# Kernel tuning notes

Hardware: AMD Instinct MI355X
Metric: run time of the kernel (lower is better)

Reference implementation:

```python
import jax, jax.numpy as jnp
import numpy as np

RADIUS = 0.1
DILATION = 0.05
KERNEL_SIZE = 3  # per dim, ndim=3 -> ncells=27
NDIM = 3


def _cell_offsets():
    # Kernel cell center offsets relative to the query location.
    idx = jnp.stack(jnp.meshgrid(*([jnp.arange(KERNEL_SIZE)] * NDIM), indexing='ij'), axis=-1)
    idx = idx.reshape(-1, NDIM).astype(jnp.float32)  # [ncells, D]
    return (idx - (KERNEL_SIZE - 1) / 2.0) * DILATION


def setup_inputs() -> dict:
    key = jax.random.key(0)
    k1, k2, k3, k4, k5, k6 = jax.random.split(key, 6)
    B, N, M, K, C, O = 2, 8192, 8192, 32, 16, 16
    ncells = KERNEL_SIZE ** NDIM
    qlocs = jax.random.uniform(k1, (B, M, NDIM), dtype=jnp.float32)
    locs = jax.random.uniform(k2, (B, N, NDIM), dtype=jnp.float32)
    data = jax.random.normal(k3, (B, N, C), dtype=jnp.float32)
    neighbors = jax.random.randint(k4, (B, M, K), 0, N, dtype=jnp.int32)
    weight = jax.random.normal(k5, (O, C, ncells), dtype=jnp.float32) * 0.1
    bias = jax.random.normal(k6, (O,), dtype=jnp.float32) * 0.1
    return {"qlocs": qlocs, "locs": locs, "data": data,
            "neighbors": neighbors, "weight": weight, "bias": bias}


def reference(qlocs, locs, data, neighbors, weight, bias):
    # qlocs: [B,M,D], locs: [B,N,D], data: [B,N,C]
    # neighbors: [B,M,K] (-1 padded), weight: [O,C,ncells], bias: [O]
    valid = neighbors >= 0                      # [B,M,K]
    nid = jnp.where(valid, neighbors, 0)
    # Gather neighbor locations/features per batch.
    nlocs = jax.vmap(lambda l, n: l[n])(locs, nid)   # [B,M,K,D]
    ndata = jax.vmap(lambda d, n: d[n])(data, nid)   # [B,M,K,C]

    off = _cell_offsets()                            # [ncells, D]
    # Cell centers around each query point: [B,M,ncells,D]
    centers = qlocs[:, :, None, :] + off[None, None, :, :]
    # Distance from each cell center to each neighbor: [B,M,ncells,K]
    diff = centers[:, :, :, None, :] - nlocs[:, :, None, :, :]
    d = jnp.sqrt(jnp.sum(diff * diff, axis=-1) + 1e-12)
    q = d / RADIUS
    # 'default' SPH smoothing kernel: compact support, (1 - d/H)^3 inside radius.
    kv = jnp.where((q < 1.0) & valid[:, :, None, :], (1.0 - q) ** 3, 0.0)  # [B,M,ncells,K]

    # Per-cell SPH-weighted feature accumulation: [B,M,C,ncells]
    acc = jnp.einsum('bmek,bmkc->bmce', kv, ndata)
    # Contract with conv weights: [B,M,O]
    out = jnp.einsum('bmce,oce->bmo', acc, weight) + bias[None, None, :]
    return out
```

## Files before the change

kernel.cpp:

```cpp
#include <hip/hip_runtime.h>
#include <math.h>

#define NP 8192
#define KN 32
#define CH 16
#define OCH 16
#define NCELL 27
#define EPAD 36

#define THR2 0.0349f

__global__ __launch_bounds__(1024, 8) void convsp_kernel(
    const float* __restrict__ qlocs,
    const float* __restrict__ locs,
    const float* __restrict__ data,
    const int*   __restrict__ neighbors,
    const float* __restrict__ weight,
    const float* __restrict__ bias,
    float* __restrict__ out)
{
    __shared__ float  wlds[OCH * CH * EPAD];
    __shared__ float4 offs4[32];

    const int tid  = threadIdx.x;
    const int lane = tid & 63;
    const int c    = lane & 15;
    const int h    = lane >> 4;
    const int pt   = blockIdx.x * 16 + (tid >> 6);
    const int b    = pt >> 13;

    int   nid = neighbors[pt * KN + (lane & 31)];
    float qx = qlocs[pt * 3 + 0];
    float qy = qlocs[pt * 3 + 1];
    float qz = qlocs[pt * 3 + 2];

    for (int idx = tid; idx < OCH * CH * NCELL; idx += 1024) {
        int row = idx / NCELL;
        int e   = idx - row * NCELL;
        wlds[row * EPAD + e] = weight[idx];
    }
    for (int idx = tid; idx < OCH * CH * 9; idx += 1024) {
        int row = idx / 9;
        int e   = 27 + (idx - row * 9);
        wlds[row * EPAD + e] = 0.0f;
    }
    if (tid < 32) {
        int e = tid;
        float ox = (e < NCELL) ? (float)(e / 9 - 1) * 0.05f : 0.0f;
        float oy = (e < NCELL) ? (float)((e / 3) % 3 - 1) * 0.05f : 0.0f;
        float oz = (e < NCELL) ? (float)(e % 3 - 1) * 0.05f : 0.0f;
        offs4[tid] = make_float4(ox, oy, oz, 0.0f);
    }

    int gaddr = (b * NP + max(nid, 0)) * 3;
    float lx = locs[gaddr], ly = locs[gaddr + 1], lz = locs[gaddr + 2];

    __syncthreads();

    float dx = qx - lx, dy = qy - ly, dz = qz - lz;
    bool hit = (nid >= 0) && (dx * dx + dy * dy + dz * dz < THR2);
    unsigned int mask = (unsigned int)__ballot(hit);

    float acc[8];
    #pragma unroll
    for (int i = 0; i < 8; ++i) acc[i] = 0.0f;

    const float4* otab = &offs4[h * 8];

    unsigned int mrem = mask;
    while (mrem) {
        int k = __builtin_ctz(mrem);
        mrem &= mrem - 1;

        int   nk = __shfl(nid, k, 64);
        float nx = __shfl(lx,  k, 64);
        float ny = __shfl(ly,  k, 64);
        float nz = __shfl(lz,  k, 64);

        float ndc = data[(b * NP + nk) * CH + c];

        float dqx = qx - nx, dqy = qy - ny, dqz = qz - nz;

        const float4* ot = otab;
        asm volatile("" : "+v"(ot));

        #pragma unroll
        for (int i = 0; i < 8; ++i) {
            float4 o4 = ot[i];
            float ex = dqx + o4.x, ey = dqy + o4.y, ez = dqz + o4.z;
            float t = fmaf(ex, ex, fmaf(ey, ey, ez * ez)) + 1e-12f;
            float u = fmaxf(fmaf(-10.0f, __builtin_amdgcn_sqrtf(t), 1.0f), 0.0f);
            acc[i] += (u * u) * (u * ndc);
        }
    }

    float r = 0.0f;
    if (mask) {
        const float* wrow = &wlds[c * EPAD + h * 8];

        float vv[8];
        #pragma unroll
        for (int j = 0; j < 8; ++j) {
            const float4* wA = (const float4*)(wrow + (2 * j)     * CH * EPAD);
            const float4* wB = (const float4*)(wrow + (2 * j + 1) * CH * EPAD);
            float4 a0 = wA[0], a1 = wA[1];
            float4 b0 = wB[0], b1 = wB[1];
            float pA = a0.x*acc[0] + a0.y*acc[1] + a0.z*acc[2] + a0.w*acc[3]
                     + a1.x*acc[4] + a1.y*acc[5] + a1.z*acc[6] + a1.w*acc[7];
            float pB = b0.x*acc[0] + b0.y*acc[1] + b0.z*acc[2] + b0.w*acc[3]
                     + b1.x*acc[4] + b1.y*acc[5] + b1.z*acc[6] + b1.w*acc[7];
            int bit = c & 1;
            float keep = bit ? pB : pA;
            float send = bit ? pA : pB;
            vv[j] = keep + __shfl_xor(send, 1, 64);
        }
        #pragma unroll
        for (int i = 1; i < 4; ++i) {
            int bit = (c >> i) & 1;
            #pragma unroll
            for (int j = 0; j < (8 >> i); ++j) {
                float keep = bit ? vv[2 * j + 1] : vv[2 * j];
                float send = bit ? vv[2 * j]     : vv[2 * j + 1];
                vv[j] = keep + __shfl_xor(send, 1 << i, 64);
            }
        }
        r = vv[0];
        r += __shfl_xor(r, 16, 64);
        r += __shfl_xor(r, 32, 64);
    }

    if (h == 0) out[pt * OCH + c] = r + bias[c];
}

extern "C" void kernel_launch(void* const* d_in, const int* in_sizes, int n_in,
                              void* d_out, int out_size, void* d_ws, size_t ws_size,
                              hipStream_t stream) {
    const float* qlocs     = (const float*)d_in[0];
    const float* locs      = (const float*)d_in[1];
    const float* data      = (const float*)d_in[2];
    const int*   neighbors = (const int*)d_in[3];
    const float* weight    = (const float*)d_in[4];
    const float* bias      = (const float*)d_in[5];
    float*       out       = (float*)d_out;

    const int BM = in_sizes[0] / 3;
    dim3 grid(BM / 16), block(1024);
    hipLaunchKernelGGL(convsp_kernel, grid, block, 0, stream,
                       qlocs, locs, data, neighbors, weight, bias, out);
}
```

Before: 21.25 us.

## Halve block size, vectorize weight staging, and hoist cell offsets into registers

Block size drops from 1024 to 512 threads, so each block handles 8 points instead of 16 and twice as many blocks launch. The weight copy into shared memory now uses float4 global loads. The cell offsets are read once into registers instead of from shared memory on every neighbor iteration, and bias is loaded early. The smaller blocks mean each block loads the full weight table for half as many points, and the extra per-lane offset registers may lower occupancy.

Measured after the change: 20.91 us. No clear change (-1.6%).

```diff
diff --git a/kernel.cpp b/kernel.cpp
--- a/kernel.cpp
+++ b/kernel.cpp
@@ -10,7 +10,7 @@
 
 #define THR2 0.0349f
 
-__global__ __launch_bounds__(1024, 8) void convsp_kernel(
+__global__ __launch_bounds__(512, 6) void convsp_kernel(
     const float* __restrict__ qlocs,
     const float* __restrict__ locs,
     const float* __restrict__ data,
@@ -26,20 +26,29 @@
     const int lane = tid & 63;
     const int c    = lane & 15;
     const int h    = lane >> 4;
-    const int pt   = blockIdx.x * 16 + (tid >> 6);
+    const int pt   = blockIdx.x * 8 + (tid >> 6);
     const int b    = pt >> 13;
 
     int   nid = neighbors[pt * KN + (lane & 31)];
     float qx = qlocs[pt * 3 + 0];
     float qy = qlocs[pt * 3 + 1];
     float qz = qlocs[pt * 3 + 2];
+    float bi = bias[c];
 
-    for (int idx = tid; idx < OCH * CH * NCELL; idx += 1024) {
-        int row = idx / NCELL;
-        int e   = idx - row * NCELL;
-        wlds[row * EPAD + e] = weight[idx];
+    const float4* w4g = (const float4*)weight;
+    for (int idx = tid; idx < (OCH * CH * NCELL) / 4; idx += 512) {
+        float4 w = w4g[idx];
+        int f = idx * 4;
+        int r0 = (f + 0) / NCELL, e0 = (f + 0) - r0 * NCELL;
+        int r1 = (f + 1) / NCELL, e1 = (f + 1) - r1 * NCELL;
+        int r2 = (f + 2) / NCELL, e2 = (f + 2) - r2 * NCELL;
+        int r3 = (f + 3) / NCELL, e3 = (f + 3) - r3 * NCELL;
+        wlds[r0 * EPAD + e0] = w.x;
+        wlds[r1 * EPAD + e1] = w.y;
+        wlds[r2 * EPAD + e2] = w.z;
+        wlds[r3 * EPAD + e3] = w.w;
     }
-    for (int idx = tid; idx < OCH * CH * 9; idx += 1024) {
+    for (int idx = tid; idx < OCH * CH * 9; idx += 512) {
         int row = idx / 9;
         int e   = 27 + (idx - row * 9);
         wlds[row * EPAD + e] = 0.0f;
@@ -57,6 +66,13 @@
 
     __syncthreads();
 
+    float oxr[8], oyr[8], ozr[8];
+    #pragma unroll
+    for (int i = 0; i < 8; ++i) {
+        float4 o4 = offs4[h * 8 + i];
+        oxr[i] = o4.x; oyr[i] = o4.y; ozr[i] = o4.z;
+    }
+
     float dx = qx - lx, dy = qy - ly, dz = qz - lz;
     bool hit = (nid >= 0) && (dx * dx + dy * dy + dz * dz < THR2);
     unsigned int mask = (unsigned int)__ballot(hit);
@@ -64,8 +80,6 @@
     float acc[8];
     #pragma unroll
     for (int i = 0; i < 8; ++i) acc[i] = 0.0f;
-
-    const float4* otab = &offs4[h * 8];
 
     unsigned int mrem = mask;
     while (mrem) {
@@ -81,13 +95,9 @@
 
         float dqx = qx - nx, dqy = qy - ny, dqz = qz - nz;
 
-        const float4* ot = otab;
-        asm volatile("" : "+v"(ot));
-
         #pragma unroll
         for (int i = 0; i < 8; ++i) {
-            float4 o4 = ot[i];
-            float ex = dqx + o4.x, ey = dqy + o4.y, ez = dqz + o4.z;
+            float ex = dqx + oxr[i], ey = dqy + oyr[i], ez = dqz + ozr[i];
             float t = fmaf(ex, ex, fmaf(ey, ey, ez * ez)) + 1e-12f;
             float u = fmaxf(fmaf(-10.0f, __builtin_amdgcn_sqrtf(t), 1.0f), 0.0f);
             acc[i] += (u * u) * (u * ndc);
@@ -129,7 +139,7 @@
         r += __shfl_xor(r, 32, 64);
     }
 
-    if (h == 0) out[pt * OCH + c] = r + bias[c];
+    if (h == 0) out[pt * OCH + c] = r + bi;
 }
 
 extern "C" void kernel_launch(void* const* d_in, const int* in_sizes, int n_in,
@@ -144,7 +154,7 @@
     float*       out       = (float*)d_out;
 
     const int BM = in_sizes[0] / 3;
-    dim3 grid(BM / 16), block(1024);
+    dim3 grid(BM / 8), block(512);
     hipLaunchKernelGGL(convsp_kernel, grid, block, 0, stream,
                        qlocs, locs, data, neighbors, weight, bias, out);
 }
```
